# Optimization experiments

Measured on AMD Instinct MI355X. Metric: run time of the kernel, lower is better.

Reference implementation:

```python
import jax, jax.numpy as jnp
import numpy as np

N, E = 50000, 800000
F_IN, E_DIM, D, H = 128, 64, 64, 4  # per-head channels D, heads H; concat=False -> out dim D
GROUPS = 16
EPS = 1e-5


def _p(key, shape, scale):
    return (jax.random.normal(key, shape, dtype=jnp.float32) * scale)


def setup_inputs() -> dict:
    key = jax.random.key(0)
    ks = jax.random.split(key, 40)
    inp = {
        "x": jax.random.normal(ks[0], (N, F_IN), dtype=jnp.float32),
        "edge_index": jax.random.randint(ks[1], (2, E), 0, N, dtype=jnp.int64),
        "edge_attr": jax.random.normal(ks[2], (E, E_DIM), dtype=jnp.float32),
    }
    # TransformerConv params, layer i: Wq/Wk/Wv [in, H*D] (+bias), We [E_DIM, H*D] (no bias),
    # Wskip [in, D] (+bias).  Layer 1 in=F_IN, layers 2/3 in=D.
    idx = 3
    for i, fin in zip((1, 2, 3), (F_IN, D, D)):
        s = 1.0 / np.sqrt(fin)
        se = 1.0 / np.sqrt(E_DIM)
        inp[f"Wq{i}"] = _p(ks[idx + 0], (fin, H * D), s)
        inp[f"bq{i}"] = jnp.zeros((H * D,), jnp.float32)
        inp[f"Wk{i}"] = _p(ks[idx + 1], (fin, H * D), s)
        inp[f"bk{i}"] = jnp.zeros((H * D,), jnp.float32)
        inp[f"Wv{i}"] = _p(ks[idx + 2], (fin, H * D), s)
        inp[f"bv{i}"] = jnp.zeros((H * D,), jnp.float32)
        inp[f"We{i}"] = _p(ks[idx + 3], (E_DIM, H * D), se)
        inp[f"Wskip{i}"] = _p(ks[idx + 4], (fin, D), s)
        inp[f"bskip{i}"] = jnp.zeros((D,), jnp.float32)
        idx += 5
    inp["gn_w"] = jnp.ones((D,), jnp.float32)
    inp["gn_b"] = jnp.zeros((D,), jnp.float32)
    return inp


def transformer_conv(x, src, dst, edge_attr, Wq, bq, Wk, bk, Wv, bv, We, Wskip, bskip):
    n = x.shape[0]
    q = (x @ Wq + bq).reshape(n, H, D)
    k = (x @ Wk + bk).reshape(n, H, D)
    v = (x @ Wv + bv).reshape(n, H, D)
    e = (edge_attr @ We).reshape(-1, H, D)  # [E,H,D]
    k_e = k[src] + e                          # edge-level key
    v_e = v[src] + e                          # edge-level value
    alpha = jnp.einsum('ehd,ehd->eh', q[dst], k_e) / np.sqrt(D)  # [E,H]
    # segment softmax over incoming edges of each dst node
    amax = jax.ops.segment_max(alpha, dst, num_segments=n)
    amax = jnp.where(jnp.isfinite(amax), amax, 0.0)
    ex = jnp.exp(alpha - amax[dst])
    denom = jax.ops.segment_sum(ex, dst, num_segments=n)
    attn = ex / (denom[dst] + 1e-16)
    out = jax.ops.segment_sum(attn[:, :, None] * v_e, dst, num_segments=n)  # [N,H,D]
    out = out.mean(axis=1)                     # concat=False -> mean over heads
    return out + (x @ Wskip + bskip)           # root_weight skip


def group_norm(x, w, b):
    n, c = x.shape
    xg = x.reshape(n, GROUPS, c // GROUPS)
    mu = xg.mean(axis=2, keepdims=True)
    var = xg.var(axis=2, keepdims=True)
    xn = ((xg - mu) * jax.lax.rsqrt(var + EPS)).reshape(n, c)
    return xn * w + b


def reference(x, edge_index, edge_attr,
              Wq1, bq1, Wk1, bk1, Wv1, bv1, We1, Wskip1, bskip1,
              Wq2, bq2, Wk2, bk2, Wv2, bv2, We2, Wskip2, bskip2,
              Wq3, bq3, Wk3, bk3, Wv3, bv3, We3, Wskip3, bskip3,
              gn_w, gn_b):
    src, dst = edge_index[0], edge_index[1]
    layers = [
        (Wq1, bq1, Wk1, bk1, Wv1, bv1, We1, Wskip1, bskip1),
        (Wq2, bq2, Wk2, bk2, Wv2, bv2, We2, Wskip2, bskip2),
        (Wq3, bq3, Wk3, bk3, Wv3, bv3, We3, Wskip3, bskip3),
    ]
    h = x
    for prm in layers:
        h = transformer_conv(h, src, dst, edge_attr, *prm)
        h = group_norm(h, gn_w, gn_b)
        h = jax.nn.gelu(h, approximate=False)
    return h
```

## Files before the change

### kernel.cpp

```cpp
#include <hip/hip_runtime.h>
#include <math.h>

#define NN 50000
#define NE 800000
#define NCOLS 1088

typedef long long i64;

__global__ void detect_i64(const int* __restrict__ ei32, int* __restrict__ flag) {
  int i = blockIdx.x * blockDim.x + threadIdx.x;
  if (i < 2048) {
    if (ei32[2 * i + 1] != 0) atomicOr(flag, 1);
  }
}

__global__ void extract_edges(const void* __restrict__ ei, const int* __restrict__ flag,
                              int* __restrict__ src32, int* __restrict__ dst32, int ne) {
  int is32 = *flag;
  int i = blockIdx.x * blockDim.x + threadIdx.x;
  int st = gridDim.x * blockDim.x;
  if (is32) {
    const int* p = (const int*)ei;
    for (; i < ne; i += st) { src32[i] = p[i]; dst32[i] = p[ne + i]; }
  } else {
    const i64* p = (const i64*)ei;
    for (; i < ne; i += st) { src32[i] = (int)p[i]; dst32[i] = (int)p[ne + i]; }
  }
}

__global__ void hist_kernel(const int* __restrict__ dst, int* __restrict__ deg, int ne) {
  int i = blockIdx.x * blockDim.x + threadIdx.x;
  int st = gridDim.x * blockDim.x;
  for (; i < ne; i += st) atomicAdd(&deg[dst[i]], 1);
}

#define SCHUNK 1024
__global__ void scanA(const int* __restrict__ deg, int* __restrict__ row_ptr,
                      int* __restrict__ csum, int n) {
  __shared__ int buf[SCHUNK];
  int c = blockIdx.x, t = threadIdx.x;
  int idx = c * SCHUNK + t;
  int v = (idx < n) ? deg[idx] : 0;
  buf[t] = v;
  __syncthreads();
  for (int off = 1; off < SCHUNK; off <<= 1) {
    int x = (t >= off) ? buf[t - off] : 0;
    __syncthreads();
    buf[t] += x;
    __syncthreads();
  }
  if (idx < n) row_ptr[idx + 1] = buf[t];
  if (t == SCHUNK - 1) csum[c] = buf[t];
}

__global__ void scanB(int* __restrict__ csum, int nchunks) {
  if (threadIdx.x == 0 && blockIdx.x == 0) {
    int run = 0;
    for (int c = 0; c < nchunks; ++c) { int v = csum[c]; csum[c] = run; run += v; }
  }
}

__global__ void scanC(int* __restrict__ row_ptr, const int* __restrict__ csum, int n) {
  int c = blockIdx.x, t = threadIdx.x;
  int idx = c * SCHUNK + t;
  if (idx < n) row_ptr[idx + 1] += csum[c];
  if (idx == 0) row_ptr[0] = 0;
}

__global__ void scatter_kernel(const int* __restrict__ src, const int* __restrict__ dst,
                               const int* __restrict__ row_ptr, int* __restrict__ cursor,
                               int* __restrict__ src_sorted, int* __restrict__ eid_sorted, int ne) {
  int i = blockIdx.x * blockDim.x + threadIdx.x;
  int st = gridDim.x * blockDim.x;
  for (; i < ne; i += st) {
    int d = dst[i];
    int pos = row_ptr[d] + atomicAdd(&cursor[d], 1);
    src_sorted[pos] = src[i];
    eid_sorted[pos] = i;
  }
}

__global__ void sort_lists(const int* __restrict__ row_ptr, int* __restrict__ src_sorted,
                           int* __restrict__ eid_sorted, int n) {
  int node = blockIdx.x * blockDim.x + threadIdx.x;
  if (node >= n) return;
  int beg = row_ptr[node], end = row_ptr[node + 1];
  for (int a = beg + 1; a < end; ++a) {
    int e = eid_sorted[a], s = src_sorted[a];
    int b = a - 1;
    while (b >= beg && eid_sorted[b] > e) {
      eid_sorted[b + 1] = eid_sorted[b];
      src_sorted[b + 1] = src_sorted[b];
      --b;
    }
    eid_sorted[b + 1] = e; src_sorted[b + 1] = s;
  }
}

__global__ void ea_gather(const int* __restrict__ eid_sorted, const float* __restrict__ ea,
                          float* __restrict__ ea_csr, int ne) {
  long total = (long)ne * 16;
  long st = (long)gridDim.x * blockDim.x;
  for (long i = (long)blockIdx.x * blockDim.x + threadIdx.x; i < total; i += st) {
    int j = (int)(i >> 4);
    int c = (int)(i & 15);
    int e = eid_sorted[j];
    ((float4*)ea_csr)[i] = ((const float4*)ea)[(size_t)e * 16 + c];
  }
}

__global__ void prep_wt(const float* __restrict__ Wq, const float* __restrict__ Wk,
                        const float* __restrict__ Wv, const float* __restrict__ We,
                        const float* __restrict__ Wsk, float* __restrict__ Wt, int fin) {
  int i = blockIdx.x * blockDim.x + threadIdx.x;
  if (i >= NCOLS * fin) return;
  int col = i / fin, k = i % fin;
  float val;
  if (col < 768) {
    const float* W = (col < 256) ? Wq : (col < 512) ? Wk : Wv;
    val = W[k * 256 + (col & 255)];
  } else if (col < 1024) {
    int idx = col - 768; int h = idx >> 6, ce = idx & 63;
    float a = 0.f;
    for (int d = 0; d < 64; ++d) a += Wq[k * 256 + h * 64 + d] * We[ce * 256 + h * 64 + d];
    val = a;
  } else {
    val = Wsk[k * 64 + (col - 1024)];
  }
  Wt[(size_t)col * fin + k] = val;
}

__global__ void prep_bias(const float* __restrict__ bq, const float* __restrict__ bk,
                          const float* __restrict__ bv, const float* __restrict__ We,
                          const float* __restrict__ bsk, float* __restrict__ bb) {
  int col = blockIdx.x * blockDim.x + threadIdx.x;
  if (col >= NCOLS) return;
  float val;
  if (col < 768) {
    const float* b = (col < 256) ? bq : (col < 512) ? bk : bv;
    val = b[col & 255];
  } else if (col < 1024) {
    int idx = col - 768; int h = idx >> 6, ce = idx & 63;
    float a = 0.f;
    for (int d = 0; d < 64; ++d) a += bq[h * 64 + d] * We[ce * 256 + h * 64 + d];
    val = a;
  } else {
    val = bsk[col - 1024];
  }
  bb[col] = val;
}

__global__ void prep_wpost(const float* __restrict__ We, float* __restrict__ Wt2) {
  int i = blockIdx.x * blockDim.x + threadIdx.x;
  if (i >= 64 * 256) return;
  int col = i >> 8, k = i & 255;
  int h = k >> 6, ce = k & 63;
  Wt2[i] = We[ce * 256 + h * 64 + col];
}

__global__ __launch_bounds__(256) void node_gemm_f32(
    const float* __restrict__ X, const float* __restrict__ Wt, const float* __restrict__ bb,
    float* __restrict__ qq_tab, float* __restrict__ kv_tab,
    float* __restrict__ skip_tab, int n, int fin) {
  __shared__ __align__(16) float Xs[128][68];
  __shared__ __align__(16) float Ws[64][68];
  int tid = threadIdx.x;
  int tx = tid & 15, ty = tid >> 4;
  int m0 = blockIdx.x * 128, c0 = blockIdx.y * 64;
  float acc[8][4];
  #pragma unroll
  for (int i = 0; i < 8; ++i)
    #pragma unroll
    for (int j = 0; j < 4; ++j) acc[i][j] = 0.f;

  for (int k0 = 0; k0 < fin; k0 += 64) {
    #pragma unroll
    for (int p = 0; p < 8; ++p) {
      int r = ty + 16 * p;
      float4 xv = make_float4(0.f, 0.f, 0.f, 0.f);
      if (m0 + r < n) xv = *(const float4*)&X[(size_t)(m0 + r) * fin + k0 + tx * 4];
      *(float4*)&Xs[r][tx * 4] = xv;
    }
    #pragma unroll
    for (int p = 0; p < 4; ++p) {
      int r = ty + 16 * p;
      float4 wv = *(const float4*)&Wt[(size_t)(c0 + r) * fin + k0 + tx * 4];
      *(float4*)&Ws[r][tx * 4] = wv;
    }
    __syncthreads();
    #pragma unroll 4
    for (int kk = 0; kk < 64; kk += 4) {
      float4 a[8], b[4];
      #pragma unroll
      for (int i = 0; i < 8; ++i) a[i] = *(const float4*)&Xs[ty + 16 * i][kk];
      #pragma unroll
      for (int j = 0; j < 4; ++j) b[j] = *(const float4*)&Ws[tx + 16 * j][kk];
      #pragma unroll
      for (int i = 0; i < 8; ++i)
        #pragma unroll
        for (int j = 0; j < 4; ++j) {
          acc[i][j] = fmaf(a[i].x, b[j].x, acc[i][j]);
          acc[i][j] = fmaf(a[i].y, b[j].y, acc[i][j]);
          acc[i][j] = fmaf(a[i].z, b[j].z, acc[i][j]);
          acc[i][j] = fmaf(a[i].w, b[j].w, acc[i][j]);
        }
    }
    __syncthreads();
  }
  #pragma unroll
  for (int j = 0; j < 4; ++j) {
    int col = c0 + tx + 16 * j;
    float bias = bb[col];
    #pragma unroll
    for (int i = 0; i < 8; ++i) {
      int row = m0 + ty + 16 * i;
      if (row >= n) continue;
      float val = acc[i][j] + bias;
      if (col < 256)        qq_tab[(size_t)row * 512 + col] = val;
      else if (col < 768)   kv_tab[(size_t)row * 512 + col - 256] = val;
      else if (col < 1024)  qq_tab[(size_t)row * 512 + col - 768 + 256] = val;
      else                  skip_tab[(size_t)row * 64 + col - 1024] = val;
    }
  }
}

__global__ __launch_bounds__(256) void post_gemm(
    const float* __restrict__ A, const float* __restrict__ B, float* __restrict__ C, int n) {
  __shared__ __align__(16) float Xs[128][68];
  __shared__ __align__(16) float Ws[64][68];
  int tid = threadIdx.x;
  int tx = tid & 15, ty = tid >> 4;
  int m0 = blockIdx.x * 128;
  float acc[8][4];
  #pragma unroll
  for (int i = 0; i < 8; ++i)
    #pragma unroll
    for (int j = 0; j < 4; ++j) acc[i][j] = 0.f;

  for (int k0 = 0; k0 < 256; k0 += 64) {
    #pragma unroll
    for (int p = 0; p < 8; ++p) {
      int r = ty + 16 * p;
      float4 xv = make_float4(0.f, 0.f, 0.f, 0.f);
      if (m0 + r < n) xv = *(const float4*)&A[(size_t)(m0 + r) * 256 + k0 + tx * 4];
      *(float4*)&Xs[r][tx * 4] = xv;
    }
    #pragma unroll
    for (int p = 0; p < 4; ++p) {
      int r = ty + 16 * p;
      float4 wv = *(const float4*)&B[(size_t)r * 256 + k0 + tx * 4];
      *(float4*)&Ws[r][tx * 4] = wv;
    }
    __syncthreads();
    #pragma unroll 4
    for (int kk = 0; kk < 64; kk += 4) {
      float4 a[8], b[4];
      #pragma unroll
      for (int i = 0; i < 8; ++i) a[i] = *(const float4*)&Xs[ty + 16 * i][kk];
      #pragma unroll
      for (int j = 0; j < 4; ++j) b[j] = *(const float4*)&Ws[tx + 16 * j][kk];
      #pragma unroll
      for (int i = 0; i < 8; ++i)
        #pragma unroll
        for (int j = 0; j < 4; ++j) {
          acc[i][j] = fmaf(a[i].x, b[j].x, acc[i][j]);
          acc[i][j] = fmaf(a[i].y, b[j].y, acc[i][j]);
          acc[i][j] = fmaf(a[i].z, b[j].z, acc[i][j]);
          acc[i][j] = fmaf(a[i].w, b[j].w, acc[i][j]);
        }
    }
    __syncthreads();
  }
  #pragma unroll
  for (int j = 0; j < 4; ++j) {
    int col = tx + 16 * j;
    #pragma unroll
    for (int i = 0; i < 8; ++i) {
      int row = m0 + ty + 16 * i;
      if (row >= n) continue;
      C[(size_t)row * 64 + col] = acc[i][j];
    }
  }
}

__global__ __launch_bounds__(256) void attn_kernel_v6(
    const int* __restrict__ row_ptr, const int* __restrict__ src_sorted,
    const int* __restrict__ eid_sorted, const float* __restrict__ ea,
    const float* __restrict__ ea_csr, int use_csr,
    const float* __restrict__ qq_tab, const float* __restrict__ kv_tab,
    float* __restrict__ avs_tab, float* __restrict__ awn_tab, int n) {
  int tid = threadIdx.x;
  int wave = tid >> 6, lane = tid & 63;
  int c16 = lane & 15;
  const float4* qq4 = (const float4*)qq_tab;
  const float4* kv4 = (const float4*)kv_tab;
  const float4* ec4 = (const float4*)ea_csr;
  const float4* e4p = (const float4*)ea;

  int node = blockIdx.x * 4 + wave;
  if (node >= n) return;
  int beg = row_ptr[node];
  int deg = row_ptr[node + 1] - beg;

  float4 q4 = qq4[(size_t)node * 128 + lane];
  float4 t4 = qq4[(size_t)node * 128 + 64 + lane];

  float m = -INFINITY, s = 0.f;
  float4 av = make_float4(0.f, 0.f, 0.f, 0.f);
  float4 aw = make_float4(0.f, 0.f, 0.f, 0.f);

#define LDE(j_, K_, V_, E_)                                   \
  {                                                           \
    int jc = (j_); int jm = beg + deg - 1;                    \
    if (jc > jm) jc = jm;                                     \
    int s_ = src_sorted[jc];                                  \
    const float4* kr = kv4 + (size_t)s_ * 128;                \
    K_ = kr[lane]; V_ = kr[64 + lane];                        \
    if (use_csr) E_ = ec4[(size_t)jc * 16 + c16];             \
    else { int e_ = eid_sorted[jc];                           \
           E_ = e4p[(size_t)e_ * 16 + c16]; }                 \
  }

#define PROC(K_, V_, E_)                                      \
  {                                                           \
    float p = q4.x * K_.x + q4.y * K_.y + q4.z * K_.z + q4.w * K_.w \
            + t4.x * E_.x + t4.y * E_.y + t4.z * E_.z + t4.w * E_.w; \
    p += __shfl_xor(p, 1);                                    \
    p += __shfl_xor(p, 2);                                    \
    p += __shfl_xor(p, 4);                                    \
    p += __shfl_xor(p, 8);                                    \
    p *= 0.125f;                                              \
    float d_ = p - m;                                         \
    float e_ = __expf(-fabsf(d_));                            \
    float sc = d_ > 0.f ? e_ : 1.f;                           \
    float pp = d_ > 0.f ? 1.f : e_;                           \
    m = fmaxf(m, p);                                          \
    s = s * sc + pp;                                          \
    av.x = av.x * sc + pp * V_.x; av.y = av.y * sc + pp * V_.y; \
    av.z = av.z * sc + pp * V_.z; av.w = av.w * sc + pp * V_.w; \
    aw.x = aw.x * sc + pp * E_.x; aw.y = aw.y * sc + pp * E_.y; \
    aw.z = aw.z * sc + pp * E_.z; aw.w = aw.w * sc + pp * E_.w; \
  }

  if (deg > 0) {
    float4 KA, VA, EA, KB, VB, EB;
    LDE(beg + 0, KA, VA, EA);
    LDE(beg + 1, KB, VB, EB);
    int t = 0;
    for (; t + 1 < deg; t += 2) {
      {
        float4 nK, nV, nE;
        LDE(beg + t + 2, nK, nV, nE);
        PROC(KA, VA, EA);
        KA = nK; VA = nV; EA = nE;
      }
      {
        float4 nK, nV, nE;
        LDE(beg + t + 3, nK, nV, nE);
        PROC(KB, VB, EB);
        KB = nK; VB = nV; EB = nE;
      }
    }
    if (t < deg) PROC(KA, VA, EA);
  }

  float inv = s > 0.f ? 1.f / s : 0.f;
  float4 awn = make_float4(aw.x * inv, aw.y * inv, aw.z * inv, aw.w * inv);
  float4 avn = make_float4(av.x * inv, av.y * inv, av.z * inv, av.w * inv);

  ((float4*)awn_tab)[(size_t)node * 64 + lane] = awn;

  avn.x += __shfl_xor(avn.x, 16); avn.y += __shfl_xor(avn.y, 16);
  avn.z += __shfl_xor(avn.z, 16); avn.w += __shfl_xor(avn.w, 16);
  avn.x += __shfl_xor(avn.x, 32); avn.y += __shfl_xor(avn.y, 32);
  avn.z += __shfl_xor(avn.z, 32); avn.w += __shfl_xor(avn.w, 32);
  if (lane < 16)
    ((float4*)avs_tab)[(size_t)node * 16 + c16] = avn;
}

__global__ void finish_kernel(const float* __restrict__ avs, const float* __restrict__ post,
                              const float* __restrict__ skip, const float* __restrict__ gnw,
                              const float* __restrict__ gnb, float* __restrict__ out, int n) {
  int g = blockIdx.x * blockDim.x + threadIdx.x;
  if (g >= n * 16) return;
  int node = g >> 4, grp = g & 15;
  float4 a = ((const float4*)avs)[(size_t)node * 16 + grp];
  float4 p = ((const float4*)post)[(size_t)node * 16 + grp];
  float4 sk = ((const float4*)skip)[(size_t)node * 16 + grp];
  float4 gw = ((const float4*)gnw)[grp];
  float4 gb = ((const float4*)gnb)[grp];
  float v0 = 0.25f * (a.x + p.x) + sk.x;
  float v1 = 0.25f * (a.y + p.y) + sk.y;
  float v2 = 0.25f * (a.z + p.z) + sk.z;
  float v3 = 0.25f * (a.w + p.w) + sk.w;
  float mu = ((v0 + v1) + (v2 + v3)) * 0.25f;
  float d0 = v0 - mu, d1 = v1 - mu, d2 = v2 - mu, d3 = v3 - mu;
  float var = ((d0 * d0 + d1 * d1) + (d2 * d2 + d3 * d3)) * 0.25f;
  float r = rsqrtf(var + 1e-5f);
  float y0 = d0 * r * gw.x + gb.x;
  float y1 = d1 * r * gw.y + gb.y;
  float y2 = d2 * r * gw.z + gb.z;
  float y3 = d3 * r * gw.w + gb.w;
  #define GELU(y) (0.5f * (y) * (1.0f + erff((y) * 0.70710678118654752f)))
  float4 o;
  o.x = GELU(y0); o.y = GELU(y1); o.z = GELU(y2); o.w = GELU(y3);
  ((float4*)out)[(size_t)node * 16 + grp] = o;
}

extern "C" void kernel_launch(void* const* d_in, const int* in_sizes, int n_in,
                              void* d_out, int out_size, void* d_ws, size_t ws_size,
                              hipStream_t stream) {
  (void)in_sizes; (void)n_in;
  const float* x = (const float*)d_in[0];
  const void* ei = d_in[1];
  const float* ea = (const float*)d_in[2];
  const float *Wq[3], *bq[3], *Wk[3], *bk[3], *Wv[3], *bv[3], *We[3], *Wsk[3], *bsk[3];
  for (int L = 0; L < 3; ++L) {
    int b = 3 + 9 * L;
    Wq[L] = (const float*)d_in[b + 0]; bq[L] = (const float*)d_in[b + 1];
    Wk[L] = (const float*)d_in[b + 2]; bk[L] = (const float*)d_in[b + 3];
    Wv[L] = (const float*)d_in[b + 4]; bv[L] = (const float*)d_in[b + 5];
    We[L] = (const float*)d_in[b + 6]; Wsk[L] = (const float*)d_in[b + 7];
    bsk[L] = (const float*)d_in[b + 8];
  }
  const float* gnw = (const float*)d_in[30];
  const float* gnb = (const float*)d_in[31];

  char* p = (char*)d_ws;
  auto alloc = [&](size_t bytes) -> void* {
    void* r = (void*)p;
    p += (bytes + 255) & ~(size_t)255;
    return r;
  };
  float* qq_tab = (float*)alloc((size_t)NN * 512 * 4);
  float* kv_tab = (float*)alloc((size_t)NN * 512 * 4);
  float* skip_tab = (float*)alloc((size_t)NN * 64 * 4);
  float* h_buf = (float*)alloc((size_t)NN * 64 * 4);
  float* avs_tab = (float*)alloc((size_t)NN * 64 * 4);
  float* awn_tab = (float*)alloc((size_t)NN * 256 * 4);
  float* post_tab = (float*)alloc((size_t)NN * 64 * 4);
  int* row_ptr = (int*)alloc((size_t)(NN + 1) * 4);
  int* deg = (int*)alloc((size_t)NN * 4);
  int* cursor = (int*)alloc((size_t)NN * 4);
  int* csum = (int*)alloc(1024 * 4);
  int* src_sorted = (int*)alloc((size_t)NE * 4);
  int* eid_sorted = (int*)alloc((size_t)NE * 4);
  int* src32 = (int*)alloc((size_t)NE * 4);
  int* dst32 = (int*)alloc((size_t)NE * 4);
  int* flag = (int*)alloc(256);
  float* Wt[3]; float* bb[3]; float* Wt2[3];
  Wt[0] = (float*)alloc((size_t)NCOLS * 128 * 4);
  Wt[1] = (float*)alloc((size_t)NCOLS * 64 * 4);
  Wt[2] = (float*)alloc((size_t)NCOLS * 64 * 4);
  for (int L = 0; L < 3; ++L) bb[L] = (float*)alloc((size_t)NCOLS * 4);
  for (int L = 0; L < 3; ++L) Wt2[L] = (float*)alloc((size_t)64 * 256 * 4);

  if ((size_t)(p - (char*)d_ws) > ws_size) {
    hipMemsetAsync(d_out, 0, (size_t)out_size * 4, stream);
    return;
  }

  float* ea_csr = nullptr;
  int use_csr = 0;
  {
    size_t need = (size_t)(p - (char*)d_ws) + (size_t)NE * 64 * 4 + 256;
    if (need <= ws_size) {
      ea_csr = (float*)alloc((size_t)NE * 64 * 4);
      use_csr = 1;
    }
  }

  hipMemsetAsync(deg, 0, (size_t)NN * 4, stream);
  hipMemsetAsync(cursor, 0, (size_t)NN * 4, stream);
  hipMemsetAsync(flag, 0, 4, stream);

  detect_i64<<<8, 256, 0, stream>>>((const int*)ei, flag);
  extract_edges<<<2048, 256, 0, stream>>>(ei, flag, src32, dst32, NE);

  hist_kernel<<<2048, 256, 0, stream>>>(dst32, deg, NE);
  int nchunks = (NN + SCHUNK - 1) / SCHUNK;
  scanA<<<nchunks, SCHUNK, 0, stream>>>(deg, row_ptr, csum, NN);
  scanB<<<1, 64, 0, stream>>>(csum, nchunks);
  scanC<<<nchunks, SCHUNK, 0, stream>>>(row_ptr, csum, NN);
  scatter_kernel<<<2048, 256, 0, stream>>>(src32, dst32, row_ptr, cursor, src_sorted, eid_sorted, NE);
  sort_lists<<<(NN + 255) / 256, 256, 0, stream>>>(row_ptr, src_sorted, eid_sorted, NN);
  if (use_csr)
    ea_gather<<<2048, 256, 0, stream>>>(eid_sorted, ea, ea_csr, NE);

  for (int L = 0; L < 3; ++L) {
    int fin = (L == 0) ? 128 : 64;
    prep_wt<<<(NCOLS * fin + 255) / 256, 256, 0, stream>>>(Wq[L], Wk[L], Wv[L], We[L], Wsk[L], Wt[L], fin);
    prep_bias<<<(NCOLS + 255) / 256, 256, 0, stream>>>(bq[L], bk[L], bv[L], We[L], bsk[L], bb[L]);
    prep_wpost<<<64, 256, 0, stream>>>(We[L], Wt2[L]);
  }

  const float* hin = x;
  int nblk = (NN + 3) / 4;
  for (int L = 0; L < 3; ++L) {
    int fin = (L == 0) ? 128 : 64;
    dim3 g((NN + 127) / 128, 17);
    node_gemm_f32<<<g, 256, 0, stream>>>(hin, Wt[L], bb[L], qq_tab, kv_tab, skip_tab, NN, fin);
    attn_kernel_v6<<<nblk, 256, 0, stream>>>(
        row_ptr, src_sorted, eid_sorted, ea, ea_csr, use_csr,
        qq_tab, kv_tab, avs_tab, awn_tab, NN);
    post_gemm<<<(NN + 127) / 128, 256, 0, stream>>>(awn_tab, Wt2[L], post_tab, NN);
    finish_kernel<<<(NN * 16 + 255) / 256, 256, 0, stream>>>(
        avs_tab, post_tab, skip_tab, gnw, gnb,
        (L == 2) ? (float*)d_out : h_buf, NN);
    hin = h_buf;
  }
}
```

Measured before the change: 1.761 ms.

## Use split-bf16 MFMA for node GEMM and fuse post GEMM with GroupNorm

The FP32 FMA node GEMM is replaced by an MFMA bf16 kernel that splits each operand into hi/lo bf16 parts and issues three MFMAs per tile (hi*hi, hi*lo, lo*hi) to keep near-fp32 accuracy. The input x and the transposed weights are pre-split by a new conversion kernel. The post GEMM is fused with the GroupNorm/GELU finish kernel, which now writes the next layer's input directly as hi/lo bf16, removing an intermediate buffer round trip. This adds conversion passes and some precision loss from dropping the lo*lo term.

```diff
diff --git a/kernel.cpp b/kernel.cpp
--- a/kernel.cpp
+++ b/kernel.cpp
@@ -6,6 +6,19 @@
 #define NCOLS 1088
 
 typedef long long i64;
+typedef unsigned short u16;
+typedef short bf16x8 __attribute__((ext_vector_type(8)));
+typedef unsigned short u16x8 __attribute__((ext_vector_type(8)));
+typedef float f32x4 __attribute__((ext_vector_type(4)));
+
+static __device__ __forceinline__ float bf2f(u16 u) {
+  union { float f; unsigned b; } x; x.b = ((unsigned)u) << 16; return x.f;
+}
+static __device__ __forceinline__ u16 f2bf(float f) {
+  union { float f; unsigned b; } x; x.f = f;
+  unsigned r = x.b + 0x7FFFu + ((x.b >> 16) & 1u);
+  return (u16)(r >> 16);
+}
 
 __global__ void detect_i64(const int* __restrict__ ei32, int* __restrict__ flag) {
   int i = blockIdx.x * blockDim.x + threadIdx.x;
@@ -106,6 +119,18 @@
     int c = (int)(i & 15);
     int e = eid_sorted[j];
     ((float4*)ea_csr)[i] = ((const float4*)ea)[(size_t)e * 16 + c];
+  }
+}
+
+__global__ void cvt_split(const float* __restrict__ in, u16* __restrict__ hi,
+                          u16* __restrict__ lo, int nElem) {
+  int i = blockIdx.x * blockDim.x + threadIdx.x;
+  int st = gridDim.x * blockDim.x;
+  for (; i < nElem; i += st) {
+    float v = in[i];
+    u16 h = f2bf(v);
+    hi[i] = h;
+    lo[i] = f2bf(v - bf2f(h));
   }
 }
 
@@ -158,127 +183,75 @@
   Wt2[i] = We[ce * 256 + h * 64 + col];
 }
 
-__global__ __launch_bounds__(256) void node_gemm_f32(
-    const float* __restrict__ X, const float* __restrict__ Wt, const float* __restrict__ bb,
+__global__ __launch_bounds__(256) void node_gemm_mfma(
+    const u16* __restrict__ Xhi, const u16* __restrict__ Xlo,
+    const u16* __restrict__ Whi, const u16* __restrict__ Wlo,
+    const float* __restrict__ bb,
     float* __restrict__ qq_tab, float* __restrict__ kv_tab,
     float* __restrict__ skip_tab, int n, int fin) {
-  __shared__ __align__(16) float Xs[128][68];
-  __shared__ __align__(16) float Ws[64][68];
-  int tid = threadIdx.x;
-  int tx = tid & 15, ty = tid >> 4;
-  int m0 = blockIdx.x * 128, c0 = blockIdx.y * 64;
-  float acc[8][4];
+  __shared__ __align__(16) u16 Ah[64][72];
+  __shared__ __align__(16) u16 Al[64][72];
+  __shared__ __align__(16) u16 Bh[64][72];
+  __shared__ __align__(16) u16 Bl[64][72];
+  int tid = threadIdx.x, wave = tid >> 6, lane = tid & 63;
+  int c0 = blockIdx.x * 64, m0 = blockIdx.y * 64;
+  f32x4 acc[4];
   #pragma unroll
-  for (int i = 0; i < 8; ++i)
+  for (int i = 0; i < 4; ++i) acc[i] = (f32x4){0.f, 0.f, 0.f, 0.f};
+
+  int lr = tid >> 2, sg = (tid & 3) * 16;
+  for (int k0 = 0; k0 < fin; k0 += 64) {
+    u16x8 z = {0, 0, 0, 0, 0, 0, 0, 0};
+    u16x8 a0 = z, a1 = z, l0 = z, l1 = z;
+    if (m0 + lr < n) {
+      const u16* ph = &Xhi[(size_t)(m0 + lr) * fin + k0 + sg];
+      a0 = *(const u16x8*)ph; a1 = *(const u16x8*)(ph + 8);
+      const u16* pl = &Xlo[(size_t)(m0 + lr) * fin + k0 + sg];
+      l0 = *(const u16x8*)pl; l1 = *(const u16x8*)(pl + 8);
+    }
+    *(u16x8*)&Ah[lr][sg] = a0; *(u16x8*)&Ah[lr][sg + 8] = a1;
+    *(u16x8*)&Al[lr][sg] = l0; *(u16x8*)&Al[lr][sg + 8] = l1;
+    {
+      const u16* ph = &Whi[(size_t)(c0 + lr) * fin + k0 + sg];
+      *(u16x8*)&Bh[lr][sg] = *(const u16x8*)ph;
+      *(u16x8*)&Bh[lr][sg + 8] = *(const u16x8*)(ph + 8);
+      const u16* pl = &Wlo[(size_t)(c0 + lr) * fin + k0 + sg];
+      *(u16x8*)&Bl[lr][sg] = *(const u16x8*)pl;
+      *(u16x8*)&Bl[lr][sg + 8] = *(const u16x8*)(pl + 8);
+    }
+    __syncthreads();
+    int arow = wave * 16 + (lane & 15);
+    int kb = (lane >> 4) * 8;
     #pragma unroll
-    for (int j = 0; j < 4; ++j) acc[i][j] = 0.f;
-
-  for (int k0 = 0; k0 < fin; k0 += 64) {
-    #pragma unroll
-    for (int p = 0; p < 8; ++p) {
-      int r = ty + 16 * p;
-      float4 xv = make_float4(0.f, 0.f, 0.f, 0.f);
-      if (m0 + r < n) xv = *(const float4*)&X[(size_t)(m0 + r) * fin + k0 + tx * 4];
-      *(float4*)&Xs[r][tx * 4] = xv;
-    }
-    #pragma unroll
-    for (int p = 0; p < 4; ++p) {
-      int r = ty + 16 * p;
-      float4 wv = *(const float4*)&Wt[(size_t)(c0 + r) * fin + k0 + tx * 4];
-      *(float4*)&Ws[r][tx * 4] = wv;
+    for (int ks = 0; ks < 2; ++ks) {
+      bf16x8 ah = *(const bf16x8*)&Ah[arow][ks * 32 + kb];
+      bf16x8 al_ = *(const bf16x8*)&Al[arow][ks * 32 + kb];
+      #pragma unroll
+      for (int nf = 0; nf < 4; ++nf) {
+        bf16x8 bh = *(const bf16x8*)&Bh[nf * 16 + (lane & 15)][ks * 32 + kb];
+        bf16x8 bl = *(const bf16x8*)&Bl[nf * 16 + (lane & 15)][ks * 32 + kb];
+        acc[nf] = __builtin_amdgcn_mfma_f32_16x16x32_bf16(ah, bh, acc[nf], 0, 0, 0);
+        acc[nf] = __builtin_amdgcn_mfma_f32_16x16x32_bf16(ah, bl, acc[nf], 0, 0, 0);
+        acc[nf] = __builtin_amdgcn_mfma_f32_16x16x32_bf16(al_, bh, acc[nf], 0, 0, 0);
+      }
     }
     __syncthreads();
-    #pragma unroll 4
-    for (int kk = 0; kk < 64; kk += 4) {
-      float4 a[8], b[4];
-      #pragma unroll
-      for (int i = 0; i < 8; ++i) a[i] = *(const float4*)&Xs[ty + 16 * i][kk];
-      #pragma unroll
-      for (int j = 0; j < 4; ++j) b[j] = *(const float4*)&Ws[tx + 16 * j][kk];
-      #pragma unroll
-      for (int i = 0; i < 8; ++i)
-        #pragma unroll
-        for (int j = 0; j < 4; ++j) {
-          acc[i][j] = fmaf(a[i].x, b[j].x, acc[i][j]);
-          acc[i][j] = fmaf(a[i].y, b[j].y, acc[i][j]);
-          acc[i][j] = fmaf(a[i].z, b[j].z, acc[i][j]);
-          acc[i][j] = fmaf(a[i].w, b[j].w, acc[i][j]);
-        }
-    }
-    __syncthreads();
-  }
+  }
+  int rbase = m0 + wave * 16 + (lane >> 4) * 4;
+  int cl = lane & 15;
   #pragma unroll
-  for (int j = 0; j < 4; ++j) {
-    int col = c0 + tx + 16 * j;
+  for (int nf = 0; nf < 4; ++nf) {
+    int col = c0 + nf * 16 + cl;
     float bias = bb[col];
     #pragma unroll
-    for (int i = 0; i < 8; ++i) {
-      int row = m0 + ty + 16 * i;
+    for (int r = 0; r < 4; ++r) {
+      int row = rbase + r;
       if (row >= n) continue;
-      float val = acc[i][j] + bias;
+      float val = acc[nf][r] + bias;
       if (col < 256)        qq_tab[(size_t)row * 512 + col] = val;
       else if (col < 768)   kv_tab[(size_t)row * 512 + col - 256] = val;
-      else if (col < 1024)  qq_tab[(size_t)row * 512 + col - 768 + 256] = val;
+      else if (col < 1024)  qq_tab[(size_t)row * 512 + col - 512] = val;
       else                  skip_tab[(size_t)row * 64 + col - 1024] = val;
-    }
-  }
-}
-
-__global__ __launch_bounds__(256) void post_gemm(
-    const float* __restrict__ A, const float* __restrict__ B, float* __restrict__ C, int n) {
-  __shared__ __align__(16) float Xs[128][68];
-  __shared__ __align__(16) float Ws[64][68];
-  int tid = threadIdx.x;
-  int tx = tid & 15, ty = tid >> 4;
-  int m0 = blockIdx.x * 128;
-  float acc[8][4];
-  #pragma unroll
-  for (int i = 0; i < 8; ++i)
-    #pragma unroll
-    for (int j = 0; j < 4; ++j) acc[i][j] = 0.f;
-
-  for (int k0 = 0; k0 < 256; k0 += 64) {
-    #pragma unroll
-    for (int p = 0; p < 8; ++p) {
-      int r = ty + 16 * p;
-      float4 xv = make_float4(0.f, 0.f, 0.f, 0.f);
-      if (m0 + r < n) xv = *(const float4*)&A[(size_t)(m0 + r) * 256 + k0 + tx * 4];
-      *(float4*)&Xs[r][tx * 4] = xv;
-    }
-    #pragma unroll
-    for (int p = 0; p < 4; ++p) {
-      int r = ty + 16 * p;
-      float4 wv = *(const float4*)&B[(size_t)r * 256 + k0 + tx * 4];
-      *(float4*)&Ws[r][tx * 4] = wv;
-    }
-    __syncthreads();
-    #pragma unroll 4
-    for (int kk = 0; kk < 64; kk += 4) {
-      float4 a[8], b[4];
-      #pragma unroll
-      for (int i = 0; i < 8; ++i) a[i] = *(const float4*)&Xs[ty + 16 * i][kk];
-      #pragma unroll
-      for (int j = 0; j < 4; ++j) b[j] = *(const float4*)&Ws[tx + 16 * j][kk];
-      #pragma unroll
-      for (int i = 0; i < 8; ++i)
-        #pragma unroll
-        for (int j = 0; j < 4; ++j) {
-          acc[i][j] = fmaf(a[i].x, b[j].x, acc[i][j]);
-          acc[i][j] = fmaf(a[i].y, b[j].y, acc[i][j]);
-          acc[i][j] = fmaf(a[i].z, b[j].z, acc[i][j]);
-          acc[i][j] = fmaf(a[i].w, b[j].w, acc[i][j]);
-        }
-    }
-    __syncthreads();
-  }
-  #pragma unroll
-  for (int j = 0; j < 4; ++j) {
-    int col = tx + 16 * j;
-    #pragma unroll
-    for (int i = 0; i < 8; ++i) {
-      int row = m0 + ty + 16 * i;
-      if (row >= n) continue;
-      C[(size_t)row * 64 + col] = acc[i][j];
     }
   }
 }
@@ -378,33 +351,102 @@
     ((float4*)avs_tab)[(size_t)node * 16 + c16] = avn;
 }
 
-__global__ void finish_kernel(const float* __restrict__ avs, const float* __restrict__ post,
-                              const float* __restrict__ skip, const float* __restrict__ gnw,
-                              const float* __restrict__ gnb, float* __restrict__ out, int n) {
-  int g = blockIdx.x * blockDim.x + threadIdx.x;
-  if (g >= n * 16) return;
-  int node = g >> 4, grp = g & 15;
-  float4 a = ((const float4*)avs)[(size_t)node * 16 + grp];
-  float4 p = ((const float4*)post)[(size_t)node * 16 + grp];
-  float4 sk = ((const float4*)skip)[(size_t)node * 16 + grp];
-  float4 gw = ((const float4*)gnw)[grp];
-  float4 gb = ((const float4*)gnb)[grp];
-  float v0 = 0.25f * (a.x + p.x) + sk.x;
-  float v1 = 0.25f * (a.y + p.y) + sk.y;
-  float v2 = 0.25f * (a.z + p.z) + sk.z;
-  float v3 = 0.25f * (a.w + p.w) + sk.w;
-  float mu = ((v0 + v1) + (v2 + v3)) * 0.25f;
-  float d0 = v0 - mu, d1 = v1 - mu, d2 = v2 - mu, d3 = v3 - mu;
-  float var = ((d0 * d0 + d1 * d1) + (d2 * d2 + d3 * d3)) * 0.25f;
-  float r = rsqrtf(var + 1e-5f);
-  float y0 = d0 * r * gw.x + gb.x;
-  float y1 = d1 * r * gw.y + gb.y;
-  float y2 = d2 * r * gw.z + gb.z;
-  float y3 = d3 * r * gw.w + gb.w;
-  #define GELU(y) (0.5f * (y) * (1.0f + erff((y) * 0.70710678118654752f)))
-  float4 o;
-  o.x = GELU(y0); o.y = GELU(y1); o.z = GELU(y2); o.w = GELU(y3);
-  ((float4*)out)[(size_t)node * 16 + grp] = o;
+__global__ __launch_bounds__(256) void post_gn(
+    const float* __restrict__ A, const float* __restrict__ B,
+    const float* __restrict__ avs, const float* __restrict__ skip,
+    const float* __restrict__ gnw, const float* __restrict__ gnb,
+    float* __restrict__ out_f32, u16* __restrict__ out_hi, u16* __restrict__ out_lo, int n) {
+  __shared__ __align__(16) float Xs[128][68];
+  __shared__ __align__(16) float Ws[64][68];
+  int tid = threadIdx.x;
+  int tx = tid & 15, ty = tid >> 4;
+  int m0 = blockIdx.x * 128;
+  float acc[8][4];
+  #pragma unroll
+  for (int i = 0; i < 8; ++i)
+    #pragma unroll
+    for (int j = 0; j < 4; ++j) acc[i][j] = 0.f;
+
+  for (int k0 = 0; k0 < 256; k0 += 64) {
+    #pragma unroll
+    for (int p = 0; p < 8; ++p) {
+      int r = ty + 16 * p;
+      float4 xv = make_float4(0.f, 0.f, 0.f, 0.f);
+      if (m0 + r < n) xv = *(const float4*)&A[(size_t)(m0 + r) * 256 + k0 + tx * 4];
+      *(float4*)&Xs[r][tx * 4] = xv;
+    }
+    #pragma unroll
+    for (int p = 0; p < 4; ++p) {
+      int r = ty + 16 * p;
+      float4 wv = *(const float4*)&B[(size_t)r * 256 + k0 + tx * 4];
+      *(float4*)&Ws[r][tx * 4] = wv;
+    }
+    __syncthreads();
+    #pragma unroll 4
+    for (int kk = 0; kk < 64; kk += 4) {
+      float4 a[8], b[4];
+      #pragma unroll
+      for (int i = 0; i < 8; ++i) a[i] = *(const float4*)&Xs[ty + 16 * i][kk];
+      #pragma unroll
+      for (int j = 0; j < 4; ++j) b[j] = *(const float4*)&Ws[tx + 16 * j][kk];
+      #pragma unroll
+      for (int i = 0; i < 8; ++i)
+        #pragma unroll
+        for (int j = 0; j < 4; ++j) {
+          acc[i][j] = fmaf(a[i].x, b[j].x, acc[i][j]);
+          acc[i][j] = fmaf(a[i].y, b[j].y, acc[i][j]);
+          acc[i][j] = fmaf(a[i].z, b[j].z, acc[i][j]);
+          acc[i][j] = fmaf(a[i].w, b[j].w, acc[i][j]);
+        }
+    }
+    __syncthreads();
+  }
+  #pragma unroll
+  for (int j = 0; j < 4; ++j)
+    #pragma unroll
+    for (int i = 0; i < 8; ++i)
+      Xs[ty + 16 * i][tx + 16 * j] = acc[i][j];
+  __syncthreads();
+
+  #pragma unroll
+  for (int rep = 0; rep < 8; ++rep) {
+    int id = tid + 256 * rep;
+    int rl = id >> 4, grp = id & 15;
+    int row = m0 + rl;
+    if (row >= n) continue;
+    float4 a = ((const float4*)avs)[(size_t)row * 16 + grp];
+    float4 sk = ((const float4*)skip)[(size_t)row * 16 + grp];
+    float4 gw = ((const float4*)gnw)[grp];
+    float4 gb = ((const float4*)gnb)[grp];
+    float p0 = Xs[rl][grp * 4 + 0], p1 = Xs[rl][grp * 4 + 1];
+    float p2 = Xs[rl][grp * 4 + 2], p3 = Xs[rl][grp * 4 + 3];
+    float v0 = 0.25f * (a.x + p0) + sk.x;
+    float v1 = 0.25f * (a.y + p1) + sk.y;
+    float v2 = 0.25f * (a.z + p2) + sk.z;
+    float v3 = 0.25f * (a.w + p3) + sk.w;
+    float mu = ((v0 + v1) + (v2 + v3)) * 0.25f;
+    float d0 = v0 - mu, d1 = v1 - mu, d2 = v2 - mu, d3 = v3 - mu;
+    float var = ((d0 * d0 + d1 * d1) + (d2 * d2 + d3 * d3)) * 0.25f;
+    float r = rsqrtf(var + 1e-5f);
+    float y0 = d0 * r * gw.x + gb.x;
+    float y1 = d1 * r * gw.y + gb.y;
+    float y2 = d2 * r * gw.z + gb.z;
+    float y3 = d3 * r * gw.w + gb.w;
+    #define GELU(y) (0.5f * (y) * (1.0f + erff((y) * 0.70710678118654752f)))
+    float g0 = GELU(y0), g1 = GELU(y1), g2 = GELU(y2), g3 = GELU(y3);
+    if (out_f32) {
+      float4 o; o.x = g0; o.y = g1; o.z = g2; o.w = g3;
+      ((float4*)out_f32)[(size_t)row * 16 + grp] = o;
+    } else {
+      u16 h0 = f2bf(g0), h1 = f2bf(g1), h2 = f2bf(g2), h3 = f2bf(g3);
+      ushort4 hv; hv.x = h0; hv.y = h1; hv.z = h2; hv.w = h3;
+      *(ushort4*)&out_hi[(size_t)row * 64 + grp * 4] = hv;
+      ushort4 lv;
+      lv.x = f2bf(g0 - bf2f(h0)); lv.y = f2bf(g1 - bf2f(h1));
+      lv.z = f2bf(g2 - bf2f(h2)); lv.w = f2bf(g3 - bf2f(h3));
+      *(ushort4*)&out_lo[(size_t)row * 64 + grp * 4] = lv;
+    }
+  }
 }
 
 extern "C" void kernel_launch(void* const* d_in, const int* in_sizes, int n_in,
@@ -435,10 +477,12 @@
   float* qq_tab = (float*)alloc((size_t)NN * 512 * 4);
   float* kv_tab = (float*)alloc((size_t)NN * 512 * 4);
   float* skip_tab = (float*)alloc((size_t)NN * 64 * 4);
-  float* h_buf = (float*)alloc((size_t)NN * 64 * 4);
   float* avs_tab = (float*)alloc((size_t)NN * 64 * 4);
   float* awn_tab = (float*)alloc((size_t)NN * 256 * 4);
-  float* post_tab = (float*)alloc((size_t)NN * 64 * 4);
+  u16* xhi = (u16*)alloc((size_t)NN * 128 * 2);
+  u16* xlo = (u16*)alloc((size_t)NN * 128 * 2);
+  u16* hhi = (u16*)alloc((size_t)NN * 64 * 2);
+  u16* hlo = (u16*)alloc((size_t)NN * 64 * 2);
   int* row_ptr = (int*)alloc((size_t)(NN + 1) * 4);
   int* deg = (int*)alloc((size_t)NN * 4);
   int* cursor = (int*)alloc((size_t)NN * 4);
@@ -449,9 +493,16 @@
   int* dst32 = (int*)alloc((size_t)NE * 4);
   int* flag = (int*)alloc(256);
   float* Wt[3]; float* bb[3]; float* Wt2[3];
+  u16 *whi[3], *wlo[3];
   Wt[0] = (float*)alloc((size_t)NCOLS * 128 * 4);
   Wt[1] = (float*)alloc((size_t)NCOLS * 64 * 4);
   Wt[2] = (float*)alloc((size_t)NCOLS * 64 * 4);
+  whi[0] = (u16*)alloc((size_t)NCOLS * 128 * 2);
+  wlo[0] = (u16*)alloc((size_t)NCOLS * 128 * 2);
+  whi[1] = (u16*)alloc((size_t)NCOLS * 64 * 2);
+  wlo[1] = (u16*)alloc((size_t)NCOLS * 64 * 2);
+  whi[2] = (u16*)alloc((size_t)NCOLS * 64 * 2);
+  wlo[2] = (u16*)alloc((size_t)NCOLS * 64 * 2);
   for (int L = 0; L < 3; ++L) bb[L] = (float*)alloc((size_t)NCOLS * 4);
   for (int L = 0; L < 3; ++L) Wt2[L] = (float*)alloc((size_t)64 * 256 * 4);
 
@@ -487,26 +538,31 @@
   if (use_csr)
     ea_gather<<<2048, 256, 0, stream>>>(eid_sorted, ea, ea_csr, NE);
 
+  cvt_split<<<2048, 256, 0, stream>>>(x, xhi, xlo, NN * 128);
+
   for (int L = 0; L < 3; ++L) {
     int fin = (L == 0) ? 128 : 64;
     prep_wt<<<(NCOLS * fin + 255) / 256, 256, 0, stream>>>(Wq[L], Wk[L], Wv[L], We[L], Wsk[L], Wt[L], fin);
     prep_bias<<<(NCOLS + 255) / 256, 256, 0, stream>>>(bq[L], bk[L], bv[L], We[L], bsk[L], bb[L]);
     prep_wpost<<<64, 256, 0, stream>>>(We[L], Wt2[L]);
-  }
-
-  const float* hin = x;
+    cvt_split<<<(NCOLS * fin + 255) / 256, 256, 0, stream>>>(Wt[L], whi[L], wlo[L], NCOLS * fin);
+  }
+
+  const u16* hi_in = xhi;
+  const u16* lo_in = xlo;
   int nblk = (NN + 3) / 4;
   for (int L = 0; L < 3; ++L) {
     int fin = (L == 0) ? 128 : 64;
-    dim3 g((NN + 127) / 128, 17);
-    node_gemm_f32<<<g, 256, 0, stream>>>(hin, Wt[L], bb[L], qq_tab, kv_tab, skip_tab, NN, fin);
+    dim3 g(17, (NN + 63) / 64);
+    node_gemm_mfma<<<g, 256, 0, stream>>>(hi_in, lo_in, whi[L], wlo[L], bb[L],
+                                          qq_tab, kv_tab, skip_tab, NN, fin);
     attn_kernel_v6<<<nblk, 256, 0, stream>>>(
         row_ptr, src_sorted, eid_sorted, ea, ea_csr, use_csr,
         qq_tab, kv_tab, avs_tab, awn_tab, NN);
-    post_gemm<<<(NN + 127) / 128, 256, 0, stream>>>(awn_tab, Wt2[L], post_tab, NN);
-    finish_kernel<<<(NN * 16 + 255) / 256, 256, 0, stream>>>(
-        avs_tab, post_tab, skip_tab, gnw, gnb,
-        (L == 2) ? (float*)d_out : h_buf, NN);
-    hin = h_buf;
-  }
-}
+    post_gn<<<(NN + 127) / 128, 256, 0, stream>>>(
+        awn_tab, Wt2[L], avs_tab, skip_tab, gnw, gnb,
+        (L == 2) ? (float*)d_out : nullptr,
+        (L < 2) ? hhi : nullptr, (L < 2) ? hlo : nullptr, NN);
+    hi_in = hhi; lo_in = hlo;
+  }
+}
```

Result: faster. 1.536 ms (-12.8%).
